# Performance work log

Measured on AMD Instinct MI355X. Metric: run time of the kernel, lower is better.

The kernel has to match this reference:

```python
import jax, jax.numpy as jnp
import numpy as np

B, D_in, D_hid, D_out, D_future = 1024, 1024, 1024, 512, 32


def _lin_init(key, out_d, in_d, k_scale):
    k = 1.0 / np.sqrt(k_scale)
    k1, k2 = jax.random.split(key)
    W = jax.random.uniform(k1, (out_d, in_d), minval=-k, maxval=k, dtype=jnp.float32)
    b = jax.random.uniform(k2, (out_d,), minval=-k, maxval=k, dtype=jnp.float32)
    return W, b


def _lstm_cell(x, h, c, W_ih, W_hh, b_ih, b_hh):
    # PyTorch LSTMCell gate order: i, f, g, o
    gates = x @ W_ih.T + b_ih + h @ W_hh.T + b_hh
    i, f, g, o = jnp.split(gates, 4, axis=1)
    c2 = jax.nn.sigmoid(f) * c + jax.nn.sigmoid(i) * jnp.tanh(g)
    h2 = jax.nn.sigmoid(o) * jnp.tanh(c2)
    return h2, c2


def setup_inputs() -> dict:
    key = jax.random.key(0)
    ks = jax.random.split(key, 16)
    x = jax.random.normal(ks[0], (B, D_in), dtype=jnp.float32)
    hx = jax.random.normal(ks[1], (B, D_hid), dtype=jnp.float32)
    cx = jax.random.normal(ks[2], (B, D_hid), dtype=jnp.float32)
    # Decoder LSTMCell(D_out -> D_hid); torch init scale 1/sqrt(hidden)
    W_ih_dec, b_ih_dec = _lin_init(ks[3], 4 * D_hid, D_out, D_hid)
    W_hh_dec, b_hh_dec = _lin_init(ks[4], 4 * D_hid, D_hid, D_hid)
    W_r0, b_r0 = _lin_init(ks[5], D_hid, D_hid, D_hid)
    W_rp, b_rp = _lin_init(ks[6], D_out, D_hid, D_hid)
    W_rr, b_rr = _lin_init(ks[7], D_out, D_out, D_out)
    W_s0, b_s0 = _lin_init(ks[8], D_in, D_hid, D_hid)
    # StaRNNCell LSTMCell(2*D_in -> D_hid)
    W_ih_sta, b_ih_sta = _lin_init(ks[9], 4 * D_hid, 2 * D_in, D_hid)
    W_hh_sta, b_hh_sta = _lin_init(ks[10], 4 * D_hid, D_hid, D_hid)
    W_sn, b_sn = _lin_init(ks[11], D_out, D_hid, D_hid)
    return dict(x=x, hx=hx, cx=cx,
                W_ih_dec=W_ih_dec, W_hh_dec=W_hh_dec, b_ih_dec=b_ih_dec, b_hh_dec=b_hh_dec,
                W_r0=W_r0, b_r0=b_r0, W_rp=W_rp, b_rp=b_rp, W_rr=W_rr, b_rr=b_rr,
                W_s0=W_s0, b_s0=b_s0,
                W_ih_sta=W_ih_sta, W_hh_sta=W_hh_sta, b_ih_sta=b_ih_sta, b_hh_sta=b_hh_sta,
                W_sn=W_sn, b_sn=b_sn)


def reference(x, hx, cx,
              W_ih_dec, W_hh_dec, b_ih_dec, b_hh_dec,
              W_r0, b_r0, W_rp, b_rp, W_rr, b_rr,
              W_s0, b_s0,
              W_ih_sta, W_hh_sta, b_ih_sta, b_hh_sta,
              W_sn, b_sn):
    ohx, ocx = hx, cx
    r0 = jnp.zeros((x.shape[0], D_out), dtype=x.dtype)
    hd0 = hx @ W_r0.T + b_r0  # LinLayerR0

    def step(carry, _):
        r, hd, cd = carry
        hd, cd = _lstm_cell(r, hd, cd, W_ih_dec, W_hh_dec, b_ih_dec, b_hh_dec)
        p = hd @ W_rp.T + b_rp    # LinLayerRp
        r = p @ W_rr.T + b_rr     # LinLayerRr
        return (r, hd, cd), (hd, p)

    _, (fts_bar, Act_bar) = jax.lax.scan(step, (r0, hd0, cx), None, length=D_future)
    # fts_bar: [D_future, B, D_hid]; AvgPool1d over D_future == mean over axis 0
    hbar = fts_bar.mean(axis=0)
    xbar = jax.nn.relu(hbar @ W_s0.T + b_s0)  # LinLayerS0 + relu
    xcat = jnp.concatenate([x, xbar], axis=1)
    hx2, cx2 = _lstm_cell(xcat, ohx, ocx, W_ih_sta, W_hh_sta, b_ih_sta, b_hh_sta)
    Act = hx2 @ W_sn.T + b_sn  # LinLayerSn
    return (Act, Act_bar, (hx2, cx2))
```

## Files before the change

### kernel.cpp

```cpp
#include <hip/hip_runtime.h>
#include <hip/hip_bf16.h>
#include <stdint.h>


typedef unsigned short ushort_t;
typedef __attribute__((ext_vector_type(8))) short short8;
typedef __attribute__((ext_vector_type(4))) float floatx4;

__device__ __forceinline__ unsigned short f2bf(float f) {
    unsigned int u = __float_as_uint(f);
    u += 0x7FFF + ((u >> 16) & 1);
    return (unsigned short)(u >> 16);
}
__device__ __forceinline__ float sigm(float x) { return 1.f / (1.f + __expf(-x)); }

__device__ __forceinline__ void glds16(const ushort_t* g, const ushort_t* l) {
    __builtin_amdgcn_global_load_lds(
        (const __attribute__((address_space(1))) uint32_t*)g,
        (__attribute__((address_space(3))) uint32_t*)l, 16, 0, 0);
}

template <bool WF, bool WB, bool RELU>
__global__ __launch_bounds__(256)
void gemm_bt(const ushort_t* __restrict__ A, int lda,
             const ushort_t* __restrict__ Bw, int ldb,
             int Kloop, int kzOff,
             const float* __restrict__ bias,
             float* __restrict__ Cf, int ldcf, size_t czStride,
             ushort_t* __restrict__ Cb, int ldcb) {
    __shared__ __align__(16) ushort_t As[128 * 32];
    __shared__ __align__(16) ushort_t Bs[128 * 32];
    const int t = threadIdx.x;
    const int l = t & 63;
    const int w = t >> 6;
    const int m0 = blockIdx.y << 7;
    const int n0 = blockIdx.x << 7;
    const int kz = blockIdx.z;
    A  += (size_t)kz * kzOff;
    Bw += (size_t)kz * kzOff;
    if (WF) Cf += (size_t)kz * czStride;
    const int wm = (w >> 1) << 6;
    const int wn = (w & 1) << 6;
    const int lr = l & 15;
    const int lg = l >> 4;

    floatx4 acc[4][4] = {};

    const int srow = (w << 4) + (l >> 2);
    const int cc = ((l & 3) - ((l >> 3) & 3)) & 3;
    const int scol = cc << 3;
    const ushort_t* Ag0 = A + (size_t)(m0 + srow) * lda + scol;
    const ushort_t* Ag1 = A + (size_t)(m0 + 64 + srow) * lda + scol;
    const ushort_t* Bg0 = Bw + (size_t)(n0 + srow) * ldb + scol;
    const ushort_t* Bg1 = Bw + (size_t)(n0 + 64 + srow) * ldb + scol;
    const ushort_t* lA0 = &As[t * 8];
    const ushort_t* lA1 = &As[2048 + t * 8];
    const ushort_t* lB0 = &Bs[t * 8];
    const ushort_t* lB1 = &Bs[2048 + t * 8];

    int aoff[4], boff[4];
#pragma unroll
    for (int i = 0; i < 4; i++) {
        const int Ra = wm + i * 16 + lr;
        aoff[i] = ((Ra << 2) + ((lg + ((Ra >> 1) & 3)) & 3)) << 3;
        const int Rb = wn + i * 16 + lr;
        boff[i] = ((Rb << 2) + ((lg + ((Rb >> 1) & 3)) & 3)) << 3;
    }

    for (int kk = 0; kk < Kloop; kk += 32) {
        glds16(Ag0 + kk, lA0);
        glds16(Ag1 + kk, lA1);
        glds16(Bg0 + kk, lB0);
        glds16(Bg1 + kk, lB1);
        __syncthreads();
        short8 af[4], bfr[4];
#pragma unroll
        for (int i = 0; i < 4; i++) af[i] = *(const short8*)&As[aoff[i]];
#pragma unroll
        for (int j = 0; j < 4; j++) bfr[j] = *(const short8*)&Bs[boff[j]];
#pragma unroll
        for (int i = 0; i < 4; i++)
#pragma unroll
            for (int j = 0; j < 4; j++)
                acc[i][j] = __builtin_amdgcn_mfma_f32_16x16x32_bf16(af[i], bfr[j], acc[i][j], 0, 0, 0);
        __syncthreads();
    }

#pragma unroll
    for (int i = 0; i < 4; i++) {
#pragma unroll
        for (int j = 0; j < 4; j++) {
            const int col = n0 + wn + j * 16 + lr;
            const float bv = bias ? bias[col] : 0.f;
#pragma unroll
            for (int r = 0; r < 4; r++) {
                const int row = m0 + wm + i * 16 + lg * 4 + r;
                float v = acc[i][j][r] + bv;
                if (RELU) v = fmaxf(v, 0.f);
                if (WF) Cf[(size_t)row * ldcf + col] = v;
                if (WB) Cb[(size_t)row * ldcb + col] = f2bf(v);
            }
        }
    }
}

template <bool HSUM, bool HF>
__global__ __launch_bounds__(256)
void gates_fused(const ushort_t* __restrict__ A, int lda,
                 const ushort_t* __restrict__ WI, int K,
                 const float* __restrict__ biasI,
                 const float* __restrict__ cin, float* __restrict__ cout,
                 ushort_t* __restrict__ hbf, int ldh,
                 float* __restrict__ hsum, float* __restrict__ hf) {
    __shared__ __align__(16) ushort_t As[2][64 * 32];
    __shared__ __align__(16) ushort_t Bs[2][128 * 32];
    __shared__ __align__(16) float Cs[64 * 132];
    const int t = threadIdx.x;
    const int l = t & 63;
    const int w = t >> 6;
    const int m0 = blockIdx.y << 6;
    const int n0 = blockIdx.x << 7;
    const int u0 = blockIdx.x << 5;
    const int lr = l & 15;
    const int lg = l >> 4;

    floatx4 acc[4][2] = {};

    const int srow = t >> 2;
    const int cc = ((t & 3) - ((t >> 3) & 3)) & 3;
    const int scol = cc << 3;
    const ushort_t* Ag  = A  + (size_t)(m0 + srow) * lda + scol;
    const ushort_t* Bg0 = WI + (size_t)(n0 + srow) * K + scol;
    const ushort_t* Bg1 = WI + (size_t)(n0 + 64 + srow) * K + scol;
    const ushort_t* lAp[2]  = { &As[0][t * 8], &As[1][t * 8] };
    const ushort_t* lBp0[2] = { &Bs[0][t * 8], &Bs[1][t * 8] };
    const ushort_t* lBp1[2] = { &Bs[0][2048 + t * 8], &Bs[1][2048 + t * 8] };

    int aoff[4], boff[2];
#pragma unroll
    for (int i = 0; i < 4; i++) {
        const int Ra = i * 16 + lr;
        aoff[i] = ((Ra << 2) + ((lg + ((Ra >> 1) & 3)) & 3)) << 3;
    }
#pragma unroll
    for (int jf = 0; jf < 2; jf++) {
        const int Rb = (w << 5) + jf * 16 + lr;
        boff[jf] = ((Rb << 2) + ((lg + ((Rb >> 1) & 3)) & 3)) << 3;
    }

    auto issue = [&](int b, int kk) {
        glds16(Ag + kk, lAp[b]);
        glds16(Bg0 + kk, lBp0[b]);
        glds16(Bg1 + kk, lBp1[b]);
    };
    auto compute = [&](int b) {
        short8 af[4], bfr[2];
#pragma unroll
        for (int i = 0; i < 4; i++) af[i] = *(const short8*)&As[b][aoff[i]];
#pragma unroll
        for (int jf = 0; jf < 2; jf++) bfr[jf] = *(const short8*)&Bs[b][boff[jf]];
#pragma unroll
        for (int i = 0; i < 4; i++)
#pragma unroll
            for (int jf = 0; jf < 2; jf++)
                acc[i][jf] = __builtin_amdgcn_mfma_f32_16x16x32_bf16(af[i], bfr[jf], acc[i][jf], 0, 0, 0);
    };

    issue(0, 0);
    for (int kk = 0; kk < K; kk += 64) {
        __syncthreads();
        issue(1, kk + 32);
        compute(0);
        __syncthreads();
        if (kk + 64 < K) issue(0, kk + 64);
        compute(1);
    }

#pragma unroll
    for (int i = 0; i < 4; i++)
#pragma unroll
        for (int jf = 0; jf < 2; jf++) {
            const int colb = (w << 5) + jf * 16 + lr;
#pragma unroll
            for (int r = 0; r < 4; r++)
                Cs[(i * 16 + lg * 4 + r) * 132 + colb] = acc[i][jf][r];
        }
    __syncthreads();

#pragma unroll
    for (int p = 0; p < 8; p++) {
        const int row = p * 8 + (t >> 5);
        const int uu = t & 31;
        const float4 g4 = *(const float4*)&Cs[row * 132 + uu * 4];
        const int grow = m0 + row;
        const int gu = u0 + uu;
        const float4 b4 = *(const float4*)&biasI[gu * 4];
        const float iv = sigm(g4.x + b4.x);
        const float fv = sigm(g4.y + b4.y);
        const float gv = tanhf(g4.z + b4.z);
        const float ov = sigm(g4.w + b4.w);
        const size_t cidx = (size_t)grow * 1024 + gu;
        const float c = fv * cin[cidx] + iv * gv;
        const float h = ov * tanhf(c);
        cout[cidx] = c;
        hbf[(size_t)grow * ldh + gu] = f2bf(h);
        if (HSUM) hsum[cidx] += h;
        if (HF) hf[cidx] = h;
    }
}

__global__ void pack2_bf(ushort_t* __restrict__ dst, const float* __restrict__ s1, int K1,
                         const float* __restrict__ s2, int K2) {
    const int n = blockIdx.y;
    const int k = blockIdx.x * 256 + threadIdx.x;
    const int Kt = K1 + K2;
    float v = (k < K1) ? s1[(size_t)n * K1 + k] : s2[(size_t)n * K2 + (k - K1)];
    dst[(size_t)n * Kt + k] = f2bf(v);
}

__global__ void tpose_bf(ushort_t* __restrict__ dst, const float* __restrict__ src,
                         int R, int C) {
    const int c = blockIdx.y;
    const int r = blockIdx.x * 256 + threadIdx.x;
    dst[(size_t)c * R + r] = f2bf(src[(size_t)r * C + c]);
}

__global__ void ileave_whh_k(ushort_t* __restrict__ dst, const float* __restrict__ Whh) {
    const int rI = blockIdx.y;
    const int k = blockIdx.x * 256 + threadIdx.x;
    const int r = ((rI & 3) << 10) + (rI >> 2);
    dst[(size_t)rI * 1024 + k] = f2bf(Whh[(size_t)r * 1024 + k]);
}

__global__ void ileave_add_k(ushort_t* __restrict__ dst, const float* __restrict__ Wgf,
                             const float* __restrict__ Whh) {
    const int rI = blockIdx.y;
    const int k = blockIdx.x * 256 + threadIdx.x;
    const int r = ((rI & 3) << 10) + (rI >> 2);
    dst[(size_t)rI * 1024 + k] = f2bf(Wgf[(size_t)r * 1024 + k] + Whh[(size_t)r * 1024 + k]);
}

__global__ void ileave_sta_k(ushort_t* __restrict__ dst, const float* __restrict__ Wih,
                             const float* __restrict__ Whh) {
    const int rI = blockIdx.y;
    const int k = blockIdx.x * 256 + threadIdx.x;
    const int r = ((rI & 3) << 10) + (rI >> 2);
    float v = (k < 2048) ? Wih[(size_t)r * 2048 + k] : Whh[(size_t)r * 1024 + (k - 2048)];
    dst[(size_t)rI * 3072 + k] = f2bf(v);
}

__global__ void bias_il_k(float* __restrict__ dst, const float* __restrict__ b_ih,
                          const float* __restrict__ b_hh) {
    const int rI = blockIdx.x * 256 + threadIdx.x;
    const int r = ((rI & 3) << 10) + (rI >> 2);
    dst[rI] = b_ih[r] + b_hh[r];
}

__global__ void br2_k(float* __restrict__ br2, const float* __restrict__ Wrr,
                      const float* __restrict__ b_rp, const float* __restrict__ b_rr) {
    const int o = blockIdx.x * 256 + threadIdx.x;
    float s = b_rr[o];
    for (int m = 0; m < 512; m++) s += Wrr[o * 512 + m] * b_rp[m];
    br2[o] = s;
}

__global__ void biasg_k(float* __restrict__ dst, const float* __restrict__ Wih,
                        const float* __restrict__ b_ih, const float* __restrict__ b_hh,
                        const float* __restrict__ br2) {
    const int rI = blockIdx.x * 256 + threadIdx.x;
    const int r = ((rI & 3) << 10) + (rI >> 2);
    float s = b_ih[r] + b_hh[r];
    for (int o = 0; o < 512; o++) s += Wih[(size_t)r * 512 + o] * br2[o];
    dst[rI] = s;
}

__global__ void init_dec(const float* __restrict__ cx, float* __restrict__ cd,
                         float* __restrict__ hsum) {
    int idx = blockIdx.x * 256 + threadIdx.x;
    cd[idx] = cx[idx];
    hsum[idx] = 0.f;
}

__global__ void init_sta(const float* __restrict__ x, const float* __restrict__ hx,
                         ushort_t* __restrict__ A2) {
    int idx = blockIdx.x * 256 + threadIdx.x;
    int b = idx >> 10, j = idx & 1023;
    A2[(size_t)b * 3072 + j] = f2bf(x[idx]);
    A2[(size_t)b * 3072 + 2048 + j] = f2bf(hx[idx]);
}

__global__ void hbar_bf_k(const float* __restrict__ hsum, ushort_t* __restrict__ out) {
    int idx = blockIdx.x * 256 + threadIdx.x;
    out[idx] = f2bf(hsum[idx] * (1.f / 32.f));
}

extern "C" void kernel_launch(void* const* d_in, const int* in_sizes, int n_in,
                              void* d_out, int out_size, void* d_ws, size_t ws_size,
                              hipStream_t stream) {
    const float* x        = (const float*)d_in[0];
    const float* hx       = (const float*)d_in[1];
    const float* cx       = (const float*)d_in[2];
    const float* W_ih_dec = (const float*)d_in[3];
    const float* W_hh_dec = (const float*)d_in[4];
    const float* b_ih_dec = (const float*)d_in[5];
    const float* b_hh_dec = (const float*)d_in[6];
    const float* W_r0     = (const float*)d_in[7];
    const float* b_r0     = (const float*)d_in[8];
    const float* W_rp     = (const float*)d_in[9];
    const float* b_rp     = (const float*)d_in[10];
    const float* W_rr     = (const float*)d_in[11];
    const float* b_rr     = (const float*)d_in[12];
    const float* W_s0     = (const float*)d_in[13];
    const float* b_s0     = (const float*)d_in[14];
    const float* W_ih_sta = (const float*)d_in[15];
    const float* W_hh_sta = (const float*)d_in[16];
    const float* b_ih_sta = (const float*)d_in[17];
    const float* b_hh_sta = (const float*)d_in[18];
    const float* W_sn     = (const float*)d_in[19];
    const float* b_sn     = (const float*)d_in[20];
    float* out = (float*)d_out;

    float* Act    = out;
    float* ActBar = out + 524288;
    float* Hx2    = out + 524288 + 16777216;
    float* Cx2    = Hx2 + 1048576;

    char* ws = (char*)d_ws;
    size_t off = 0;
    auto alloc = [&](size_t bytes) -> void* {
        void* p = ws + off;
        off += (bytes + 255) & ~(size_t)255;
        return p;
    };
    const size_t SLOT = 1048576;
    ushort_t* HDall  = (ushort_t*)alloc(33ull * SLOT * 2);
    ushort_t* WgI    = (ushort_t*)alloc(4096ull * 1024 * 2);
    ushort_t* WcatSI = (ushort_t*)alloc(4096ull * 3072 * 2);
    ushort_t* Wrpb   = (ushort_t*)alloc(512ull * 1024 * 2);
    ushort_t* Wr0b   = (ushort_t*)alloc(1024ull * 1024 * 2);
    ushort_t* Ws0b   = (ushort_t*)alloc(1024ull * 1024 * 2);
    ushort_t* Wsnb   = (ushort_t*)alloc(512ull * 1024 * 2);
    float*    biasDI = (float*)alloc(4096 * 4);
    float*    biasGI = (float*)alloc(4096 * 4);
    float*    biasSI = (float*)alloc(4096 * 4);
    float*    br2    = (float*)alloc(512 * 4);
    ushort_t* Acat2  = (ushort_t*)alloc(1024ull * 3072 * 2);
    float*    cd     = (float*)alloc(1024ull * 1024 * 4);
    float*    hsum   = (float*)alloc(1024ull * 1024 * 4);
    ushort_t* hbarb  = (ushort_t*)alloc(1024ull * 1024 * 2);
    ushort_t* hx2b   = (ushort_t*)alloc(1024ull * 1024 * 2);
    if (ws_size < off) return;

    float*    Wgf    = (float*)(HDall + 1 * SLOT);
    ushort_t* Wihb   = HDall + 9 * SLOT;
    ushort_t* WrpT   = HDall + 11 * SLOT;
    ushort_t* Wrp2Tb = HDall + 11 * SLOT + 524288;
    ushort_t* Wrrb   = HDall + 12 * SLOT;
    ushort_t* WhhI   = HDall + 13 * SLOT;

    init_dec<<<4096, 256, 0, stream>>>(cx, cd, hsum);
    init_sta<<<4096, 256, 0, stream>>>(x, hx, Acat2);
    pack2_bf<<<dim3(2, 512), 256, 0, stream>>>(Wrrb, W_rr, 512, nullptr, 0);
    pack2_bf<<<dim3(2, 4096), 256, 0, stream>>>(Wihb, W_ih_dec, 512, nullptr, 0);
    pack2_bf<<<dim3(4, 512), 256, 0, stream>>>(Wrpb, W_rp, 1024, nullptr, 0);
    pack2_bf<<<dim3(4, 1024), 256, 0, stream>>>(Wr0b, W_r0, 1024, nullptr, 0);
    pack2_bf<<<dim3(4, 1024), 256, 0, stream>>>(Ws0b, W_s0, 1024, nullptr, 0);
    pack2_bf<<<dim3(4, 512), 256, 0, stream>>>(Wsnb, W_sn, 1024, nullptr, 0);
    tpose_bf<<<dim3(2, 1024), 256, 0, stream>>>(WrpT, W_rp, 512, 1024);
    ileave_whh_k<<<dim3(4, 4096), 256, 0, stream>>>(WhhI, W_hh_dec);
    bias_il_k<<<16, 256, 0, stream>>>(biasDI, b_ih_dec, b_hh_dec);
    ileave_sta_k<<<dim3(12, 4096), 256, 0, stream>>>(WcatSI, W_ih_sta, W_hh_sta);
    bias_il_k<<<16, 256, 0, stream>>>(biasSI, b_ih_sta, b_hh_sta);
    br2_k<<<2, 256, 0, stream>>>(br2, W_rr, b_rp, b_rr);
    biasg_k<<<16, 256, 0, stream>>>(biasGI, W_ih_dec, b_ih_dec, b_hh_dec, br2);

    gemm_bt<false, true, false><<<dim3(4, 8, 1), 256, 0, stream>>>(
        WrpT, 512, Wrrb, 512, 512, 0, nullptr, nullptr, 0, 0, Wrp2Tb, 512);
    gemm_bt<true, false, false><<<dim3(8, 32, 1), 256, 0, stream>>>(
        Wihb, 512, Wrp2Tb, 512, 512, 0, nullptr, Wgf, 1024, 0, nullptr, 0);
    ileave_add_k<<<dim3(4, 4096), 256, 0, stream>>>(WgI, Wgf, W_hh_dec);

    gemm_bt<false, true, false><<<dim3(8, 8, 1), 256, 0, stream>>>(
        Acat2 + 2048, 3072, Wr0b, 1024, 1024, 0, b_r0, nullptr, 0, 0, HDall, 1024);

    for (int s = 0; s < 32; s++) {
        const ushort_t* WI = (s == 0) ? WhhI : WgI;
        const float* bI = (s == 0) ? biasDI : biasGI;
        gates_fused<true, false><<<dim3(32, 16), 256, 0, stream>>>(
            HDall + (size_t)s * SLOT, 1024, WI, 1024, bI,
            cd, cd, HDall + (size_t)(s + 1) * SLOT, 1024, hsum, nullptr);
    }

    gemm_bt<true, false, false><<<dim3(4, 256, 1), 256, 0, stream>>>(
        HDall + SLOT, 1024, Wrpb, 1024, 1024, 0, b_rp, ActBar, 512, 0, nullptr, 0);

    hbar_bf_k<<<4096, 256, 0, stream>>>(hsum, hbarb);
    gemm_bt<false, true, true><<<dim3(8, 8, 1), 256, 0, stream>>>(
        hbarb, 1024, Ws0b, 1024, 1024, 0, b_s0, nullptr, 0, 0, Acat2 + 1024, 3072);

    gates_fused<false, true><<<dim3(32, 16), 256, 0, stream>>>(
        Acat2, 3072, WcatSI, 3072, biasSI, cx, Cx2, hx2b, 1024, nullptr, Hx2);

    gemm_bt<true, false, false><<<dim3(4, 8, 1), 256, 0, stream>>>(
        hx2b, 1024, Wsnb, 1024, 1024, 0, b_sn, Act, 512, 0, nullptr, 0);

    (void)in_sizes; (void)n_in; (void)out_size;
}
```

Baseline: 1.280 ms.

## Load gate weights directly to registers, drop hsum accumulation, add nontemporal stores

The gates kernel now streams weight fragments straight from global memory into registers and stages only the activation tile in LDS, aliased onto the epilogue buffer, with 128-wide K steps and two-blocks-per-CU launch bounds. The per-step fp32 read-modify-write of the hidden-state running sum is removed. The mean is instead recomputed once afterwards from the 32 stored bf16 hidden slots. Output stores to final tensors use nontemporal hints. This cuts per-step memory traffic and LDS use, at the cost of register pressure, uncoalesced direct weight loads, and averaging over bf16-rounded hidden states rather than fp32 values.

```diff
diff --git a/kernel.cpp b/kernel.cpp
--- a/kernel.cpp
+++ b/kernel.cpp
@@ -12,6 +12,9 @@
     u += 0x7FFF + ((u >> 16) & 1);
     return (unsigned short)(u >> 16);
 }
+__device__ __forceinline__ float bf2f(unsigned short u) {
+    return __uint_as_float(((unsigned int)u) << 16);
+}
 __device__ __forceinline__ float sigm(float x) { return 1.f / (1.f + __expf(-x)); }
 
 __device__ __forceinline__ void glds16(const ushort_t* g, const ushort_t* l) {
@@ -20,7 +23,7 @@
         (__attribute__((address_space(3))) uint32_t*)l, 16, 0, 0);
 }
 
-template <bool WF, bool WB, bool RELU>
+template <bool WF, bool WB, bool RELU, bool NT>
 __global__ __launch_bounds__(256)
 void gemm_bt(const ushort_t* __restrict__ A, int lda,
              const ushort_t* __restrict__ Bw, int ldb,
@@ -97,24 +100,26 @@
                 const int row = m0 + wm + i * 16 + lg * 4 + r;
                 float v = acc[i][j][r] + bv;
                 if (RELU) v = fmaxf(v, 0.f);
-                if (WF) Cf[(size_t)row * ldcf + col] = v;
+                if (WF) {
+                    if (NT) __builtin_nontemporal_store(v, &Cf[(size_t)row * ldcf + col]);
+                    else Cf[(size_t)row * ldcf + col] = v;
+                }
                 if (WB) Cb[(size_t)row * ldcb + col] = f2bf(v);
             }
         }
     }
 }
 
-template <bool HSUM, bool HF>
-__global__ __launch_bounds__(256)
+template <bool HF, bool NT>
+__global__ __launch_bounds__(256, 2)
 void gates_fused(const ushort_t* __restrict__ A, int lda,
                  const ushort_t* __restrict__ WI, int K,
                  const float* __restrict__ biasI,
                  const float* __restrict__ cin, float* __restrict__ cout,
                  ushort_t* __restrict__ hbf, int ldh,
-                 float* __restrict__ hsum, float* __restrict__ hf) {
-    __shared__ __align__(16) ushort_t As[2][64 * 32];
-    __shared__ __align__(16) ushort_t Bs[2][128 * 32];
+                 float* __restrict__ hf) {
     __shared__ __align__(16) float Cs[64 * 132];
+    ushort_t* AsBase = (ushort_t*)Cs;
     const int t = threadIdx.x;
     const int l = t & 63;
     const int w = t >> 6;
@@ -129,52 +134,59 @@
     const int srow = t >> 2;
     const int cc = ((t & 3) - ((t >> 3) & 3)) & 3;
     const int scol = cc << 3;
-    const ushort_t* Ag  = A  + (size_t)(m0 + srow) * lda + scol;
-    const ushort_t* Bg0 = WI + (size_t)(n0 + srow) * K + scol;
-    const ushort_t* Bg1 = WI + (size_t)(n0 + 64 + srow) * K + scol;
-    const ushort_t* lAp[2]  = { &As[0][t * 8], &As[1][t * 8] };
-    const ushort_t* lBp0[2] = { &Bs[0][t * 8], &Bs[1][t * 8] };
-    const ushort_t* lBp1[2] = { &Bs[0][2048 + t * 8], &Bs[1][2048 + t * 8] };
-
-    int aoff[4], boff[2];
+    const ushort_t* Ag = A + (size_t)(m0 + srow) * lda + scol;
+
+    int aoff[4];
 #pragma unroll
     for (int i = 0; i < 4; i++) {
         const int Ra = i * 16 + lr;
         aoff[i] = ((Ra << 2) + ((lg + ((Ra >> 1) & 3)) & 3)) << 3;
     }
-#pragma unroll
-    for (int jf = 0; jf < 2; jf++) {
-        const int Rb = (w << 5) + jf * 16 + lr;
-        boff[jf] = ((Rb << 2) + ((lg + ((Rb >> 1) & 3)) & 3)) << 3;
-    }
-
-    auto issue = [&](int b, int kk) {
-        glds16(Ag + kk, lAp[b]);
-        glds16(Bg0 + kk, lBp0[b]);
-        glds16(Bg1 + kk, lBp1[b]);
+    const ushort_t* BgW[2];
+#pragma unroll
+    for (int jf = 0; jf < 2; jf++)
+        BgW[jf] = WI + (size_t)(n0 + (w << 5) + jf * 16 + lr) * K + (lg << 3);
+
+    auto issueA = [&](int b, int sp) {
+#pragma unroll
+        for (int s = 0; s < 4; s++)
+            glds16(Ag + sp * 128 + s * 32, AsBase + b * 8192 + s * 2048 + t * 8);
     };
-    auto compute = [&](int b) {
-        short8 af[4], bfr[2];
-#pragma unroll
-        for (int i = 0; i < 4; i++) af[i] = *(const short8*)&As[b][aoff[i]];
-#pragma unroll
-        for (int jf = 0; jf < 2; jf++) bfr[jf] = *(const short8*)&Bs[b][boff[jf]];
-#pragma unroll
-        for (int i = 0; i < 4; i++)
+    auto loadB = [&](short8 (&br)[4][2], int sp) {
+#pragma unroll
+        for (int s = 0; s < 4; s++)
 #pragma unroll
             for (int jf = 0; jf < 2; jf++)
-                acc[i][jf] = __builtin_amdgcn_mfma_f32_16x16x32_bf16(af[i], bfr[jf], acc[i][jf], 0, 0, 0);
+                br[s][jf] = *(const short8*)(BgW[jf] + sp * 128 + s * 32);
     };
-
-    issue(0, 0);
-    for (int kk = 0; kk < K; kk += 64) {
+    auto compute = [&](int b, short8 (&br)[4][2]) {
+#pragma unroll
+        for (int s = 0; s < 4; s++) {
+            short8 af[4];
+#pragma unroll
+            for (int i = 0; i < 4; i++)
+                af[i] = *(const short8*)(AsBase + b * 8192 + s * 2048 + aoff[i]);
+#pragma unroll
+            for (int i = 0; i < 4; i++)
+#pragma unroll
+                for (int jf = 0; jf < 2; jf++)
+                    acc[i][jf] = __builtin_amdgcn_mfma_f32_16x16x32_bf16(af[i], br[s][jf], acc[i][jf], 0, 0, 0);
+        }
+    };
+
+    short8 b0[4][2], b1[4][2];
+    const int NS = K >> 7;
+    issueA(0, 0);
+    loadB(b0, 0);
+    for (int sp = 0; sp < NS; sp += 2) {
         __syncthreads();
-        issue(1, kk + 32);
-        compute(0);
+        if (sp + 1 < NS) { issueA(1, sp + 1); loadB(b1, sp + 1); }
+        compute(0, b0);
         __syncthreads();
-        if (kk + 64 < K) issue(0, kk + 64);
-        compute(1);
-    }
+        if (sp + 2 < NS) { issueA(0, sp + 2); loadB(b0, sp + 2); }
+        compute(1, b1);
+    }
+    __syncthreads();
 
 #pragma unroll
     for (int i = 0; i < 4; i++)
@@ -202,10 +214,13 @@
         const size_t cidx = (size_t)grow * 1024 + gu;
         const float c = fv * cin[cidx] + iv * gv;
         const float h = ov * tanhf(c);
-        cout[cidx] = c;
+        if (NT) __builtin_nontemporal_store(c, &cout[cidx]);
+        else cout[cidx] = c;
         hbf[(size_t)grow * ldh + gu] = f2bf(h);
-        if (HSUM) hsum[cidx] += h;
-        if (HF) hf[cidx] = h;
+        if (HF) {
+            if (NT) __builtin_nontemporal_store(h, &hf[cidx]);
+            else hf[cidx] = h;
+        }
     }
 }
 
@@ -274,11 +289,9 @@
     dst[rI] = s;
 }
 
-__global__ void init_dec(const float* __restrict__ cx, float* __restrict__ cd,
-                         float* __restrict__ hsum) {
+__global__ void init_dec(const float* __restrict__ cx, float* __restrict__ cd) {
     int idx = blockIdx.x * 256 + threadIdx.x;
     cd[idx] = cx[idx];
-    hsum[idx] = 0.f;
 }
 
 __global__ void init_sta(const float* __restrict__ x, const float* __restrict__ hx,
@@ -289,9 +302,14 @@
     A2[(size_t)b * 3072 + 2048 + j] = f2bf(hx[idx]);
 }
 
-__global__ void hbar_bf_k(const float* __restrict__ hsum, ushort_t* __restrict__ out) {
+__global__ void hbar_from_slots(const ushort_t* __restrict__ HD1,
+                                ushort_t* __restrict__ out) {
+    const size_t SLOT = 1048576;
     int idx = blockIdx.x * 256 + threadIdx.x;
-    out[idx] = f2bf(hsum[idx] * (1.f / 32.f));
+    float s = 0.f;
+#pragma unroll 8
+    for (int t = 0; t < 32; t++) s += bf2f(HD1[(size_t)t * SLOT + idx]);
+    out[idx] = f2bf(s * (1.f / 32.f));
 }
 
 extern "C" void kernel_launch(void* const* d_in, const int* in_sizes, int n_in,
@@ -346,7 +364,6 @@
     float*    br2    = (float*)alloc(512 * 4);
     ushort_t* Acat2  = (ushort_t*)alloc(1024ull * 3072 * 2);
     float*    cd     = (float*)alloc(1024ull * 1024 * 4);
-    float*    hsum   = (float*)alloc(1024ull * 1024 * 4);
     ushort_t* hbarb  = (ushort_t*)alloc(1024ull * 1024 * 2);
     ushort_t* hx2b   = (ushort_t*)alloc(1024ull * 1024 * 2);
     if (ws_size < off) return;
@@ -358,7 +375,7 @@
     ushort_t* Wrrb   = HDall + 12 * SLOT;
     ushort_t* WhhI   = HDall + 13 * SLOT;
 
-    init_dec<<<4096, 256, 0, stream>>>(cx, cd, hsum);
+    init_dec<<<4096, 256, 0, stream>>>(cx, cd);
     init_sta<<<4096, 256, 0, stream>>>(x, hx, Acat2);
     pack2_bf<<<dim3(2, 512), 256, 0, stream>>>(Wrrb, W_rr, 512, nullptr, 0);
     pack2_bf<<<dim3(2, 4096), 256, 0, stream>>>(Wihb, W_ih_dec, 512, nullptr, 0);
@@ -374,34 +391,34 @@
     br2_k<<<2, 256, 0, stream>>>(br2, W_rr, b_rp, b_rr);
     biasg_k<<<16, 256, 0, stream>>>(biasGI, W_ih_dec, b_ih_dec, b_hh_dec, br2);
 
-    gemm_bt<false, true, false><<<dim3(4, 8, 1), 256, 0, stream>>>(
+    gemm_bt<false, true, false, false><<<dim3(4, 8, 1), 256, 0, stream>>>(
         WrpT, 512, Wrrb, 512, 512, 0, nullptr, nullptr, 0, 0, Wrp2Tb, 512);
-    gemm_bt<true, false, false><<<dim3(8, 32, 1), 256, 0, stream>>>(
+    gemm_bt<true, false, false, false><<<dim3(8, 32, 1), 256, 0, stream>>>(
         Wihb, 512, Wrp2Tb, 512, 512, 0, nullptr, Wgf, 1024, 0, nullptr, 0);
     ileave_add_k<<<dim3(4, 4096), 256, 0, stream>>>(WgI, Wgf, W_hh_dec);
 
-    gemm_bt<false, true, false><<<dim3(8, 8, 1), 256, 0, stream>>>(
+    gemm_bt<false, true, false, false><<<dim3(8, 8, 1), 256, 0, stream>>>(
         Acat2 + 2048, 3072, Wr0b, 1024, 1024, 0, b_r0, nullptr, 0, 0, HDall, 1024);
 
     for (int s = 0; s < 32; s++) {
         const ushort_t* WI = (s == 0) ? WhhI : WgI;
         const float* bI = (s == 0) ? biasDI : biasGI;
-        gates_fused<true, false><<<dim3(32, 16), 256, 0, stream>>>(
+        gates_fused<false, false><<<dim3(32, 16), 256, 0, stream>>>(
             HDall + (size_t)s * SLOT, 1024, WI, 1024, bI,
-            cd, cd, HDall + (size_t)(s + 1) * SLOT, 1024, hsum, nullptr);
-    }
-
-    gemm_bt<true, false, false><<<dim3(4, 256, 1), 256, 0, stream>>>(
+            cd, cd, HDall + (size_t)(s + 1) * SLOT, 1024, nullptr);
+    }
+
+    gemm_bt<true, false, false, true><<<dim3(4, 256, 1), 256, 0, stream>>>(
         HDall + SLOT, 1024, Wrpb, 1024, 1024, 0, b_rp, ActBar, 512, 0, nullptr, 0);
 
-    hbar_bf_k<<<4096, 256, 0, stream>>>(hsum, hbarb);
-    gemm_bt<false, true, true><<<dim3(8, 8, 1), 256, 0, stream>>>(
+    hbar_from_slots<<<4096, 256, 0, stream>>>(HDall + SLOT, hbarb);
+    gemm_bt<false, true, true, false><<<dim3(8, 8, 1), 256, 0, stream>>>(
         hbarb, 1024, Ws0b, 1024, 1024, 0, b_s0, nullptr, 0, 0, Acat2 + 1024, 3072);
 
-    gates_fused<false, true><<<dim3(32, 16), 256, 0, stream>>>(
-        Acat2, 3072, WcatSI, 3072, biasSI, cx, Cx2, hx2b, 1024, nullptr, Hx2);
-
-    gemm_bt<true, false, false><<<dim3(4, 8, 1), 256, 0, stream>>>(
+    gates_fused<true, true><<<dim3(32, 16), 256, 0, stream>>>(
+        Acat2, 3072, WcatSI, 3072, biasSI, cx, Cx2, hx2b, 1024, Hx2);
+
+    gemm_bt<true, false, false, true><<<dim3(4, 8, 1), 256, 0, stream>>>(
         hx2b, 1024, Wsnb, 1024, 1024, 0, b_sn, Act, 512, 0, nullptr, 0);
 
     (void)in_sizes; (void)n_in; (void)out_size;
```

Measured after the change: 1.234 ms. 3.6% less time.
